# Kernel optimization log

Measured on AMD Instinct MI355X. Metric: run time of the kernel, lower is better.

Reference implementation:

```python
import jax, jax.numpy as jnp
import numpy as np

N_NODES = 50000
N_EDGES = 800000
HIDDEN = 64
RES = 0.5  # args.res_layer


def setup_inputs() -> dict:
    key = jax.random.key(0)
    ks = jax.random.split(key, 9)
    s = 0.05  # scale weights to keep exp(att) stable
    return {
        "edge_index": jax.random.randint(ks[0], (2, N_EDGES), 0, N_NODES, dtype=jnp.int32),
        "adj_values": jax.random.uniform(ks[1], (N_EDGES,), dtype=jnp.float32),
        "embeds": jax.random.normal(ks[2], (N_NODES, HIDDEN), dtype=jnp.float32),
        "W1": jax.random.normal(ks[3], (HIDDEN, HIDDEN), dtype=jnp.float32) * s,
        "b1": jax.random.normal(ks[4], (HIDDEN,), dtype=jnp.float32) * s,
        "W2": jax.random.normal(ks[5], (HIDDEN, HIDDEN), dtype=jnp.float32) * s,
        "b2": jax.random.normal(ks[6], (HIDDEN,), dtype=jnp.float32) * s,
        "att_w": jax.random.normal(ks[7], (2 * HIDDEN,), dtype=jnp.float32) * s,
        "att_b": jax.random.normal(ks[8], (1,), dtype=jnp.float32) * s,
    }


def reference(edge_index, adj_values, embeds, W1, b1, W2, b2, att_w, att_b):
    n = embeds.shape[0]
    h = embeds.shape[1]
    row, col = edge_index[0], edge_index[1]
    # per-edge gather + two small linears with ReLU
    f1 = jax.nn.relu(embeds[row] @ W1 + b1)          # [E, h]
    f2 = jax.nn.relu(embeds[col] @ W2 + b2)          # [E, h]
    # attention score = Linear(concat(f1, f2)) -> split weight, avoid concat
    att = f1 @ att_w[:h] + f2 @ att_w[h:] + att_b[0]  # [E]
    exp_att = jnp.exp(att)
    # sparse row-wise softmax denominator via segment sum
    rowsum = jax.ops.segment_sum(exp_att, row, num_segments=n) + 1e-6  # [N]
    values = (exp_att / rowsum[row] + RES * adj_values) / (1.0 + RES)  # [E]
    # SpMM: out[i] = sum_{e: row[e]=i} values[e] * embeds[col[e]]
    out = jax.ops.segment_sum(values[:, None] * embeds[col], row, num_segments=n)  # [N, h]
    return values, out
```

## Files before the change

### kernel.cpp

```cpp
#include <hip/hip_runtime.h>
#include <hip/hip_bf16.h>

#define HID 64
#define RES_F 0.5f
#define SLOTS 64

typedef __attribute__((ext_vector_type(8))) short short8;
typedef __attribute__((ext_vector_type(4))) float f32x4;

__device__ __forceinline__ float lane_bcast_f(float v, int k) {
    return __builtin_bit_cast(float, __builtin_amdgcn_readlane(__builtin_bit_cast(int, v), k));
}
__device__ __forceinline__ int lane_bcast_i(int v, int k) {
    return __builtin_amdgcn_readlane(v, k);
}
__device__ __forceinline__ short f2bf(float x) {
    __hip_bfloat16 h = __float2bfloat16(x);
    return __builtin_bit_cast(short, h);
}

__global__ void __launch_bounds__(256) fused_prep_kernel(
    const float* __restrict__ embeds,
    const float* __restrict__ W1, const float* __restrict__ W2,
    const float* __restrict__ b1, const float* __restrict__ b2,
    const float* __restrict__ att_w, const float* __restrict__ att_b,
    const int* __restrict__ row, const int* __restrict__ col,
    const float* __restrict__ adj,
    int* __restrict__ cursor, int* __restrict__ edata,
    float* __restrict__ g, float* __restrict__ corr,
    __hip_bfloat16* __restrict__ embeds_bf,
    int n, int E, int nodeBlocks, int edgeBlocks)
{
    __shared__ short sW[2 * HID * HID];

    if (blockIdx.x < nodeBlocks) {
        for (int i = threadIdx.x; i < HID * HID; i += blockDim.x) {
            sW[i]             = f2bf(W1[i]);
            sW[HID * HID + i] = f2bf(W2[i]);
        }
        __syncthreads();

        const float ab = att_b[0];
        const int lane = threadIdx.x & 63;
        const int colx = lane & 15;
        const int quad = lane >> 4;

        short8 bfrag[8][2];
        float  sac[8], bc[8];
#pragma unroll
        for (int cb = 0; cb < 8; ++cb) {
            const int jp = cb * 16 + colx;
            const short* w = (jp < HID) ? (sW + jp) : (sW + HID * HID + jp - HID);
#pragma unroll
            for (int kh = 0; kh < 2; ++kh) {
                short8 f;
#pragma unroll
                for (int j = 0; j < 8; ++j) {
                    const int k = kh * 32 + quad * 8 + j;
                    f[j] = w[k * HID];
                }
                bfrag[cb][kh] = f;
            }
            sac[cb] = att_w[jp];
            bc[cb]  = (jp < HID) ? b1[jp] : b2[jp - HID];
        }

        int gwave = (blockIdx.x * blockDim.x + threadIdx.x) >> 6;
        const int nwave = (nodeBlocks * blockDim.x) >> 6;
        const int nbatch = (n + 15) >> 4;

        for (int b = gwave; b < nbatch; b += nwave) {
            const int base = b << 4;
            int mrow = base + colx;
            if (mrow >= n) mrow = n - 1;
            const float* ep = embeds + (size_t)mrow * HID;
            short8 afrag0, afrag1;
#pragma unroll
            for (int j = 0; j < 8; ++j) {
                afrag0[j] = f2bf(ep[quad * 8 + j]);
                afrag1[j] = f2bf(ep[32 + quad * 8 + j]);
            }
            {
                short8* ebf = (short8*)(embeds_bf + (size_t)mrow * HID);
                ebf[quad]     = afrag0;
                ebf[4 + quad] = afrag1;
            }

            float acc1[4] = {0.f, 0.f, 0.f, 0.f};
            float acc2[4] = {0.f, 0.f, 0.f, 0.f};
#pragma unroll
            for (int cb = 0; cb < 8; ++cb) {
                f32x4 C = {0.f, 0.f, 0.f, 0.f};
                C = __builtin_amdgcn_mfma_f32_16x16x32_bf16(afrag0, bfrag[cb][0], C, 0, 0, 0);
                C = __builtin_amdgcn_mfma_f32_16x16x32_bf16(afrag1, bfrag[cb][1], C, 0, 0, 0);
#pragma unroll
                for (int reg = 0; reg < 4; ++reg) {
                    const float v = fmaxf(C[reg] + bc[cb], 0.f) * sac[cb];
                    if (cb < 4) acc1[reg] += v; else acc2[reg] += v;
                }
            }
#pragma unroll
            for (int reg = 0; reg < 4; ++reg) {
#pragma unroll
                for (int off = 1; off < 16; off <<= 1) {
                    acc1[reg] += __shfl_xor(acc1[reg], off, 64);
                    acc2[reg] += __shfl_xor(acc2[reg], off, 64);
                }
            }
            if (colx == 0) {
#pragma unroll
                for (int reg = 0; reg < 4; ++reg) {
                    const int i = base + quad * 4 + reg;
                    if (i < n) {
                        g[i]    = __expf(acc2[reg]);
                        corr[i] = 1e-6f * __expf(-(acc1[reg] + ab));
                    }
                }
            }
        }
    } else {
        const int tid = (blockIdx.x - nodeBlocks) * blockDim.x + threadIdx.x;
        const int ts  = edgeBlocks * blockDim.x;
        for (int e = tid; e < E; e += ts) {
            const int r   = row[e];
            const int c   = col[e];
            const float aj = adj[e];
            const int p   = atomicAdd(&cursor[r], 1);
            if (p < SLOTS) {
                const unsigned aq = (unsigned)(aj * 65535.0f + 0.5f);
                edata[(size_t)r * SLOTS + p] = (int)((unsigned)c | (aq << 16));
            }
        }
    }
}

__global__ void __launch_bounds__(256) spmm_kernel(
    const int* __restrict__ cursor, const int* __restrict__ edata,
    const __hip_bfloat16* __restrict__ embeds_bf,
    const float* __restrict__ g, const float* __restrict__ corr,
    float* __restrict__ invD, float* __restrict__ out, int n)
{
    const float inv = 1.0f / (1.0f + RES_F);
    const int lane = threadIdx.x & 63;
    int r = (blockIdx.x * blockDim.x + threadIdx.x) >> 6;
    const int nwave = (gridDim.x * blockDim.x) >> 6;

    for (; r < n; r += nwave) {
        const int deg = min(cursor[r], SLOTS);
        const bool valid = lane < deg;
        int c = 0;
        float gc = 0.0f, aj = 0.0f;
        if (valid) {
            const unsigned pk = (unsigned)edata[(size_t)r * SLOTS + lane];
            c  = (int)(pk & 0xFFFFu);
            aj = (float)(pk >> 16) * (1.0f / 65535.0f);
            gc = g[c];
        }
        float G = gc;
#pragma unroll
        for (int off = 1; off < 64; off <<= 1)
            G += __shfl_xor(G, off, 64);
        const float invDr = 1.0f / (G + corr[r]);
        if (lane == 0) invD[r] = invDr;
        const float v = valid ? (gc * invDr + RES_F * aj) * inv : 0.0f;

        float acc = 0.0f;
        int j = 0;
        for (; j + 8 <= deg; j += 8) {
            const int   c0 = lane_bcast_i(c, j + 0);
            const int   c1 = lane_bcast_i(c, j + 1);
            const int   c2 = lane_bcast_i(c, j + 2);
            const int   c3 = lane_bcast_i(c, j + 3);
            const int   c4 = lane_bcast_i(c, j + 4);
            const int   c5 = lane_bcast_i(c, j + 5);
            const int   c6 = lane_bcast_i(c, j + 6);
            const int   c7 = lane_bcast_i(c, j + 7);
            const float b0 = __bfloat162float(embeds_bf[c0 * HID + lane]);
            const float b1 = __bfloat162float(embeds_bf[c1 * HID + lane]);
            const float b2 = __bfloat162float(embeds_bf[c2 * HID + lane]);
            const float b3 = __bfloat162float(embeds_bf[c3 * HID + lane]);
            const float b4 = __bfloat162float(embeds_bf[c4 * HID + lane]);
            const float b5 = __bfloat162float(embeds_bf[c5 * HID + lane]);
            const float b6 = __bfloat162float(embeds_bf[c6 * HID + lane]);
            const float b7 = __bfloat162float(embeds_bf[c7 * HID + lane]);
            acc = fmaf(lane_bcast_f(v, j + 0), b0, acc);
            acc = fmaf(lane_bcast_f(v, j + 1), b1, acc);
            acc = fmaf(lane_bcast_f(v, j + 2), b2, acc);
            acc = fmaf(lane_bcast_f(v, j + 3), b3, acc);
            acc = fmaf(lane_bcast_f(v, j + 4), b4, acc);
            acc = fmaf(lane_bcast_f(v, j + 5), b5, acc);
            acc = fmaf(lane_bcast_f(v, j + 6), b6, acc);
            acc = fmaf(lane_bcast_f(v, j + 7), b7, acc);
        }
        for (; j < deg; ++j) {
            const int   cj = lane_bcast_i(c, j);
            const float vj = lane_bcast_f(v, j);
            acc = fmaf(vj, __bfloat162float(embeds_bf[cj * HID + lane]), acc);
        }
        out[r * HID + lane] = acc;
    }
}

__global__ void __launch_bounds__(256) values_kernel(
    const int* __restrict__ row, const int* __restrict__ col,
    const float* __restrict__ adj,
    const float* __restrict__ g, const float* __restrict__ invD,
    float* __restrict__ values, int E)
{
    const int e = blockIdx.x * blockDim.x + threadIdx.x;
    if (e < E) {
        const float inv = 1.0f / (1.0f + RES_F);
        values[e] = (g[col[e]] * invD[row[e]] + RES_F * adj[e]) * inv;
    }
}

extern "C" void kernel_launch(void* const* d_in, const int* in_sizes, int n_in,
                              void* d_out, int out_size, void* d_ws, size_t ws_size,
                              hipStream_t stream)
{
    const int* edge_index = (const int*)d_in[0];
    const float* adj      = (const float*)d_in[1];
    const float* embeds   = (const float*)d_in[2];
    const float* W1       = (const float*)d_in[3];
    const float* b1       = (const float*)d_in[4];
    const float* W2       = (const float*)d_in[5];
    const float* b2       = (const float*)d_in[6];
    const float* att_w    = (const float*)d_in[7];
    const float* att_b    = (const float*)d_in[8];

    const int E = in_sizes[1];
    const int N = in_sizes[2] / HID;

    const int* row = edge_index;
    const int* col = edge_index + E;

    int*   edata  = (int*)d_ws;
    float* g      = (float*)(edata + (size_t)N * SLOTS);
    float* corr   = g + N;
    float* invD   = corr + N;
    int*   cursor = (int*)(invD + N);
    __hip_bfloat16* embeds_bf = (__hip_bfloat16*)(cursor + N);

    float* values = (float*)d_out;
    float* out    = values + E;

    (void)hipMemsetAsync(cursor, 0, (size_t)N * sizeof(int), stream);

    const int nodeBlocks = 784;
    const int edgeBlocks = 3125;
    fused_prep_kernel<<<nodeBlocks + edgeBlocks, 256, 0, stream>>>(
        embeds, W1, W2, b1, b2, att_w, att_b, row, col, adj,
        cursor, edata, g, corr, embeds_bf,
        N, E, nodeBlocks, edgeBlocks);

    spmm_kernel<<<12544, 256, 0, stream>>>(cursor, edata, embeds_bf,
                                           g, corr, invD, out, N);

    values_kernel<<<3125, 256, 0, stream>>>(row, col, adj, g, invD, values, E);
}
```

Baseline: 176.8 us.

## Fuse prep, SpMM and values kernels into one cooperative kernel with grid syncs

Merges the three kernel launches into a single cooperative launch whose phases are separated by grid-wide barriers. Grid size is derived from occupancy and capped, and all phases use grid-stride loops. This removes inter-kernel launch gaps and tail drain, at the cost of grid-sync overhead and reduced block counts per phase, which may lower latency hiding.

```diff
diff --git a/kernel.cpp b/kernel.cpp
--- a/kernel.cpp
+++ b/kernel.cpp
@@ -1,5 +1,8 @@
 #include <hip/hip_runtime.h>
 #include <hip/hip_bf16.h>
+#include <hip/hip_cooperative_groups.h>
+
+namespace cg = cooperative_groups;
 
 #define HID 64
 #define RES_F 0.5f
@@ -19,7 +22,7 @@
     return __builtin_bit_cast(short, h);
 }
 
-__global__ void __launch_bounds__(256) fused_prep_kernel(
+__global__ void __launch_bounds__(256) fused_all_kernel(
     const float* __restrict__ embeds,
     const float* __restrict__ W1, const float* __restrict__ W2,
     const float* __restrict__ b1, const float* __restrict__ b2,
@@ -27,13 +30,17 @@
     const int* __restrict__ row, const int* __restrict__ col,
     const float* __restrict__ adj,
     int* __restrict__ cursor, int* __restrict__ edata,
-    float* __restrict__ g, float* __restrict__ corr,
+    float* __restrict__ g, float* __restrict__ corr, float* __restrict__ invD,
     __hip_bfloat16* __restrict__ embeds_bf,
-    int n, int E, int nodeBlocks, int edgeBlocks)
+    float* __restrict__ values, float* __restrict__ out,
+    int n, int E, int nodeBlocks)
 {
+    cg::grid_group grid = cg::this_grid();
     __shared__ short sW[2 * HID * HID];
 
-    if (blockIdx.x < nodeBlocks) {
+    const int lane = threadIdx.x & 63;
+
+    if ((int)blockIdx.x < nodeBlocks) {
         for (int i = threadIdx.x; i < HID * HID; i += blockDim.x) {
             sW[i]             = f2bf(W1[i]);
             sW[HID * HID + i] = f2bf(W2[i]);
@@ -41,7 +48,6 @@
         __syncthreads();
 
         const float ab = att_b[0];
-        const int lane = threadIdx.x & 63;
         const int colx = lane & 15;
         const int quad = lane >> 4;
 
@@ -120,7 +126,7 @@
         }
     } else {
         const int tid = (blockIdx.x - nodeBlocks) * blockDim.x + threadIdx.x;
-        const int ts  = edgeBlocks * blockDim.x;
+        const int ts  = (gridDim.x - nodeBlocks) * blockDim.x;
         for (int e = tid; e < E; e += ts) {
             const int r   = row[e];
             const int c   = col[e];
@@ -132,85 +138,78 @@
             }
         }
     }
-}
-
-__global__ void __launch_bounds__(256) spmm_kernel(
-    const int* __restrict__ cursor, const int* __restrict__ edata,
-    const __hip_bfloat16* __restrict__ embeds_bf,
-    const float* __restrict__ g, const float* __restrict__ corr,
-    float* __restrict__ invD, float* __restrict__ out, int n)
-{
-    const float inv = 1.0f / (1.0f + RES_F);
-    const int lane = threadIdx.x & 63;
-    int r = (blockIdx.x * blockDim.x + threadIdx.x) >> 6;
-    const int nwave = (gridDim.x * blockDim.x) >> 6;
-
-    for (; r < n; r += nwave) {
-        const int deg = min(cursor[r], SLOTS);
-        const bool valid = lane < deg;
-        int c = 0;
-        float gc = 0.0f, aj = 0.0f;
-        if (valid) {
-            const unsigned pk = (unsigned)edata[(size_t)r * SLOTS + lane];
-            c  = (int)(pk & 0xFFFFu);
-            aj = (float)(pk >> 16) * (1.0f / 65535.0f);
-            gc = g[c];
-        }
-        float G = gc;
-#pragma unroll
-        for (int off = 1; off < 64; off <<= 1)
-            G += __shfl_xor(G, off, 64);
-        const float invDr = 1.0f / (G + corr[r]);
-        if (lane == 0) invD[r] = invDr;
-        const float v = valid ? (gc * invDr + RES_F * aj) * inv : 0.0f;
-
-        float acc = 0.0f;
-        int j = 0;
-        for (; j + 8 <= deg; j += 8) {
-            const int   c0 = lane_bcast_i(c, j + 0);
-            const int   c1 = lane_bcast_i(c, j + 1);
-            const int   c2 = lane_bcast_i(c, j + 2);
-            const int   c3 = lane_bcast_i(c, j + 3);
-            const int   c4 = lane_bcast_i(c, j + 4);
-            const int   c5 = lane_bcast_i(c, j + 5);
-            const int   c6 = lane_bcast_i(c, j + 6);
-            const int   c7 = lane_bcast_i(c, j + 7);
-            const float b0 = __bfloat162float(embeds_bf[c0 * HID + lane]);
-            const float b1 = __bfloat162float(embeds_bf[c1 * HID + lane]);
-            const float b2 = __bfloat162float(embeds_bf[c2 * HID + lane]);
-            const float b3 = __bfloat162float(embeds_bf[c3 * HID + lane]);
-            const float b4 = __bfloat162float(embeds_bf[c4 * HID + lane]);
-            const float b5 = __bfloat162float(embeds_bf[c5 * HID + lane]);
-            const float b6 = __bfloat162float(embeds_bf[c6 * HID + lane]);
-            const float b7 = __bfloat162float(embeds_bf[c7 * HID + lane]);
-            acc = fmaf(lane_bcast_f(v, j + 0), b0, acc);
-            acc = fmaf(lane_bcast_f(v, j + 1), b1, acc);
-            acc = fmaf(lane_bcast_f(v, j + 2), b2, acc);
-            acc = fmaf(lane_bcast_f(v, j + 3), b3, acc);
-            acc = fmaf(lane_bcast_f(v, j + 4), b4, acc);
-            acc = fmaf(lane_bcast_f(v, j + 5), b5, acc);
-            acc = fmaf(lane_bcast_f(v, j + 6), b6, acc);
-            acc = fmaf(lane_bcast_f(v, j + 7), b7, acc);
-        }
-        for (; j < deg; ++j) {
-            const int   cj = lane_bcast_i(c, j);
-            const float vj = lane_bcast_f(v, j);
-            acc = fmaf(vj, __bfloat162float(embeds_bf[cj * HID + lane]), acc);
-        }
-        out[r * HID + lane] = acc;
-    }
-}
-
-__global__ void __launch_bounds__(256) values_kernel(
-    const int* __restrict__ row, const int* __restrict__ col,
-    const float* __restrict__ adj,
-    const float* __restrict__ g, const float* __restrict__ invD,
-    float* __restrict__ values, int E)
-{
-    const int e = blockIdx.x * blockDim.x + threadIdx.x;
-    if (e < E) {
+
+    grid.sync();
+
+    {
         const float inv = 1.0f / (1.0f + RES_F);
-        values[e] = (g[col[e]] * invD[row[e]] + RES_F * adj[e]) * inv;
+        int r = (blockIdx.x * blockDim.x + threadIdx.x) >> 6;
+        const int nwave = (gridDim.x * blockDim.x) >> 6;
+
+        for (; r < n; r += nwave) {
+            const int deg = min(cursor[r], SLOTS);
+            const bool valid = lane < deg;
+            int c = 0;
+            float gc = 0.0f, aj = 0.0f;
+            if (valid) {
+                const unsigned pk = (unsigned)edata[(size_t)r * SLOTS + lane];
+                c  = (int)(pk & 0xFFFFu);
+                aj = (float)(pk >> 16) * (1.0f / 65535.0f);
+                gc = g[c];
+            }
+            float G = gc;
+#pragma unroll
+            for (int off = 1; off < 64; off <<= 1)
+                G += __shfl_xor(G, off, 64);
+            const float invDr = 1.0f / (G + corr[r]);
+            if (lane == 0) invD[r] = invDr;
+            const float v = valid ? (gc * invDr + RES_F * aj) * inv : 0.0f;
+
+            float acc = 0.0f;
+            int j = 0;
+            for (; j + 8 <= deg; j += 8) {
+                const int   c0 = lane_bcast_i(c, j + 0);
+                const int   c1 = lane_bcast_i(c, j + 1);
+                const int   c2 = lane_bcast_i(c, j + 2);
+                const int   c3 = lane_bcast_i(c, j + 3);
+                const int   c4 = lane_bcast_i(c, j + 4);
+                const int   c5 = lane_bcast_i(c, j + 5);
+                const int   c6 = lane_bcast_i(c, j + 6);
+                const int   c7 = lane_bcast_i(c, j + 7);
+                const float b0 = __bfloat162float(embeds_bf[c0 * HID + lane]);
+                const float b1 = __bfloat162float(embeds_bf[c1 * HID + lane]);
+                const float b2 = __bfloat162float(embeds_bf[c2 * HID + lane]);
+                const float b3 = __bfloat162float(embeds_bf[c3 * HID + lane]);
+                const float b4 = __bfloat162float(embeds_bf[c4 * HID + lane]);
+                const float b5 = __bfloat162float(embeds_bf[c5 * HID + lane]);
+                const float b6 = __bfloat162float(embeds_bf[c6 * HID + lane]);
+                const float b7 = __bfloat162float(embeds_bf[c7 * HID + lane]);
+                acc = fmaf(lane_bcast_f(v, j + 0), b0, acc);
+                acc = fmaf(lane_bcast_f(v, j + 1), b1, acc);
+                acc = fmaf(lane_bcast_f(v, j + 2), b2, acc);
+                acc = fmaf(lane_bcast_f(v, j + 3), b3, acc);
+                acc = fmaf(lane_bcast_f(v, j + 4), b4, acc);
+                acc = fmaf(lane_bcast_f(v, j + 5), b5, acc);
+                acc = fmaf(lane_bcast_f(v, j + 6), b6, acc);
+                acc = fmaf(lane_bcast_f(v, j + 7), b7, acc);
+            }
+            for (; j < deg; ++j) {
+                const int   cj = lane_bcast_i(c, j);
+                const float vj = lane_bcast_f(v, j);
+                acc = fmaf(vj, __bfloat162float(embeds_bf[cj * HID + lane]), acc);
+            }
+            out[r * HID + lane] = acc;
+        }
+    }
+
+    grid.sync();
+
+    {
+        const float inv = 1.0f / (1.0f + RES_F);
+        const int tid = blockIdx.x * blockDim.x + threadIdx.x;
+        const int ts  = gridDim.x * blockDim.x;
+        for (int e = tid; e < E; e += ts)
+            values[e] = (g[col[e]] * invD[row[e]] + RES_F * adj[e]) * inv;
     }
 }
 
@@ -246,15 +245,27 @@
 
     (void)hipMemsetAsync(cursor, 0, (size_t)N * sizeof(int), stream);
 
-    const int nodeBlocks = 784;
-    const int edgeBlocks = 3125;
-    fused_prep_kernel<<<nodeBlocks + edgeBlocks, 256, 0, stream>>>(
-        embeds, W1, W2, b1, b2, att_w, att_b, row, col, adj,
-        cursor, edata, g, corr, embeds_bf,
-        N, E, nodeBlocks, edgeBlocks);
-
-    spmm_kernel<<<12544, 256, 0, stream>>>(cursor, edata, embeds_bf,
-                                           g, corr, invD, out, N);
-
-    values_kernel<<<3125, 256, 0, stream>>>(row, col, adj, g, invD, values, E);
-}
+    static int coopGrid = 0;
+    if (coopGrid == 0) {
+        int perCU = 0;
+        if (hipOccupancyMaxActiveBlocksPerMultiprocessor(
+                &perCU, fused_all_kernel, 256, 0) != hipSuccess || perCU < 1)
+            perCU = 4;
+        coopGrid = perCU * 256;
+        if (coopGrid > 2048) coopGrid = 2048;
+    }
+    int nodeBlocks = coopGrid / 4;
+    if (nodeBlocks < 1) nodeBlocks = 1;
+
+    int nArg = N, eArg = E;
+    void* args[] = {
+        (void*)&embeds, (void*)&W1, (void*)&W2, (void*)&b1, (void*)&b2,
+        (void*)&att_w, (void*)&att_b, (void*)&row, (void*)&col, (void*)&adj,
+        (void*)&cursor, (void*)&edata, (void*)&g, (void*)&corr, (void*)&invD,
+        (void*)&embeds_bf, (void*)&values, (void*)&out,
+        (void*)&nArg, (void*)&eArg, (void*)&nodeBlocks
+    };
+    (void)hipLaunchCooperativeKernel((const void*)fused_all_kernel,
+                                     dim3(coopGrid), dim3(256),
+                                     args, 0, stream);
+}
```

Measured after the change: 361.1 us. 104% more time.
